# Kernel tuning notes

Measured on AMD Instinct MI355X. Metric: run time of the kernel, lower is better.

## Reference

```python
import jax, jax.numpy as jnp
import numpy as np

B, P, E, D = 256, 2048, 16, 2
HID, OUT = 128, 128
BN_EPS = 1e-5


def setup_inputs() -> dict:
    key = jax.random.key(0)
    ks = jax.random.split(key, 16)
    inp = {
        "barcode_h0": jax.random.normal(ks[0], (B, P, D), jnp.float32),
        "barcode_h0_count": jax.random.randint(ks[1], (B,), 0, P),
        "barcode_h1": jax.random.normal(ks[2], (B, P, D), jnp.float32),
        "barcode_h1_count": jax.random.randint(ks[3], (B,), 0, P),
        # SLayer params (one per homology dim): centers ~ U[0,1), log_sharpness = log(3.0)
        "centers0": jax.random.uniform(ks[4], (E, D), jnp.float32),
        "log_sharp0": jnp.full((E, D), np.log(3.0), jnp.float32),
        "centers1": jax.random.uniform(ks[5], (E, D), jnp.float32),
        "log_sharp1": jnp.full((E, D), np.log(3.0), jnp.float32),
        # head: Linear(2E -> HID, no bias), BN, ReLU, Linear(HID -> OUT, no bias), BN
        "W1": jax.random.normal(ks[6], (2 * E, HID), jnp.float32) / np.sqrt(2 * E),
        "gamma1": jnp.ones((HID,), jnp.float32),
        "beta1": jnp.zeros((HID,), jnp.float32),
        "W2": jax.random.normal(ks[7], (HID, OUT), jnp.float32) / np.sqrt(HID),
        "gamma2": jnp.ones((OUT,), jnp.float32),
        "beta2": jnp.zeros((OUT,), jnp.float32),
    }
    return inp


def _slayer(pts, counts, centers, log_sharp):
    # pts: [B,P,2], counts: [B], centers/log_sharp: [E,2]
    sharp = jax.nn.softplus(log_sharp) + 1e-6                       # [E,2]
    diff = pts[:, :, None, :] - centers[None, None, :, :]           # [B,P,E,2]
    resp = jnp.exp(-jnp.sum(sharp * diff * diff, axis=-1))          # [B,P,E]
    mask = (jnp.arange(pts.shape[1])[None, :] < counts[:, None]).astype(resp.dtype)
    return jnp.sum(resp * mask[:, :, None], axis=1)                 # [B,E]


def _batchnorm_train(x, gamma, beta):
    m = jnp.mean(x, axis=0)
    v = jnp.var(x, axis=0)  # biased, as torch uses for normalization
    return (x - m) * jax.lax.rsqrt(v + BN_EPS) * gamma + beta


def reference(barcode_h0, barcode_h0_count, barcode_h1, barcode_h1_count,
              centers0, log_sharp0, centers1, log_sharp1,
              W1, gamma1, beta1, W2, gamma2, beta2):
    f0 = _slayer(barcode_h0, barcode_h0_count, centers0, log_sharp0)  # [B,E]
    f1 = _slayer(barcode_h1, barcode_h1_count, centers1, log_sharp1)  # [B,E]
    x = jnp.concatenate([f0, f1], axis=1)                             # [B,2E]
    h = jax.nn.relu(_batchnorm_train(x @ W1, gamma1, beta1))          # [B,HID]
    y = _batchnorm_train(h @ W2, gamma2, beta2)                       # [B,OUT]
    norm = jnp.maximum(jnp.linalg.norm(y, axis=1, keepdims=True), 1e-12)
    return y / norm
```

## Files before the change

### kernel.cpp

```cpp
#include <hip/hip_runtime.h>

#define Bsz 256
#define Pn  2048
#define En  16
#define HIDn 128
#define OUTn 128
#define BN_EPS 1e-5f
#define NREP 16
#define NGRP 16
#define POISON_U 0xAAAAAAAAu

typedef unsigned int u32;
typedef unsigned long long u64;


__device__ __forceinline__ float coh_load(const float* p) {
    return __hip_atomic_load(p, __ATOMIC_RELAXED, __HIP_MEMORY_SCOPE_AGENT);
}
__device__ __forceinline__ void coh_store64(u64* p, u64 v) {
    __hip_atomic_store(p, v, __ATOMIC_RELAXED, __HIP_MEMORY_SCOPE_AGENT);
}
__device__ __forceinline__ u64 coh_load64(const u64* p) {
    return __hip_atomic_load(p, __ATOMIC_RELAXED, __HIP_MEMORY_SCOPE_AGENT);
}

__global__ __launch_bounds__(256) void k_fused(
    const float* __restrict__ pts0, const int* __restrict__ cnt0,
    const float* __restrict__ pts1, const int* __restrict__ cnt1,
    const float* __restrict__ c0, const float* __restrict__ ls0,
    const float* __restrict__ c1, const float* __restrict__ ls1,
    const float* __restrict__ W1,
    const float* __restrict__ g1, const float* __restrict__ be1,
    const float* __restrict__ W2,
    const float* __restrict__ g2, const float* __restrict__ be2,
    float* __restrict__ stats,
    u32* __restrict__ bars,
    u64* __restrict__ mstd,
    float* __restrict__ out)
{
    __shared__ float W2ld[HIDn * OUTn];
    __shared__ float4 cs[2][En];
    __shared__ float red[4][32];
    __shared__ float xrow[32];
    __shared__ float hrow[HIDn];
    __shared__ float part[4];
    __shared__ int   amFin;

    const int tid = threadIdx.x;
    const int b   = blockIdx.x;

    float* sum1R   = stats;
    float* sumsq1R = stats + NREP * HIDn;
    float* sum2R   = stats + 2 * NREP * HIDn;
    float* sumsq2R = stats + 3 * NREP * HIDn;
    const int rep = (b & (NREP - 1)) * HIDn;

    u32* leaf0 = bars + (b >> 4) * 64;
    u32* root0 = bars + 1024;
    u32* fin0  = bars + 1088;
    u32* leaf1 = bars + 2048 + (b >> 4) * 64;
    u32* root1 = bars + 3072;
    u32* fin1  = bars + 3136;
    u64* mstd1 = mstd;
    u64* mstd2 = mstd + HIDn;

    if (tid < 32) {
        int h = tid >> 4, e = tid & 15;
        const float* C = h ? c1 : c0;
        const float* L = h ? ls1 : ls0;
        float zx = L[2 * e], zy = L[2 * e + 1];
        float sx = (zx > 20.f) ? zx : logf(1.f + expf(zx));
        float sy = (zy > 20.f) ? zy : logf(1.f + expf(zy));
        cs[h][e] = make_float4(C[2 * e], C[2 * e + 1], sx + 1e-6f, sy + 1e-6f);
    }
    __syncthreads();

    const int n0 = cnt0[b];
    const int n1 = cnt1[b];
    const float4* q0 = (const float4*)(pts0 + (size_t)b * Pn * 2);
    const float4* q1 = (const float4*)(pts1 + (size_t)b * Pn * 2);

    float4 f0[4], f1[4];
    #pragma unroll
    for (int i = 0; i < 4; i++) {
        f0[i] = q0[tid + (i << 8)];
        f1[i] = q1[tid + (i << 8)];
    }
    const float4* W2v = (const float4*)W2;
    float4 w2r[16];
    #pragma unroll
    for (int i = 0; i < 16; i++) w2r[i] = W2v[tid + (i << 8)];

    float g1v = 0.f, b1v = 0.f, g2v = 0.f, b2v = 0.f;
    if (tid < HIDn) { g1v = g1[tid]; b1v = be1[tid]; g2v = g2[tid]; b2v = be2[tid]; }

    float m0a[4], m0b[4], m1a[4], m1b[4];
    #pragma unroll
    for (int i = 0; i < 4; i++) {
        int p = (tid + (i << 8)) << 1;
        m0a[i] = (p     < n0) ? 1.f : 0.f;
        m0b[i] = (p + 1 < n0) ? 1.f : 0.f;
        m1a[i] = (p     < n1) ? 1.f : 0.f;
        m1b[i] = (p + 1 < n1) ? 1.f : 0.f;
    }

    float acc0[En], acc1[En];
    #pragma unroll
    for (int e = 0; e < En; e++) { acc0[e] = 0.f; acc1[e] = 0.f; }

    #pragma unroll
    for (int e = 0; e < En; e++) {
        float4 c = cs[0][e];
        float4 d = cs[1][e];
        float a0 = acc0[e], a1 = acc1[e];
        #pragma unroll
        for (int i = 0; i < 4; i++) {
            float dx, dy;
            dx = f0[i].x - c.x; dy = f0[i].y - c.y;
            a0 = fmaf(m0a[i], __expf(-(c.z * dx * dx + c.w * dy * dy)), a0);
            dx = f0[i].z - c.x; dy = f0[i].w - c.y;
            a0 = fmaf(m0b[i], __expf(-(c.z * dx * dx + c.w * dy * dy)), a0);
            dx = f1[i].x - d.x; dy = f1[i].y - d.y;
            a1 = fmaf(m1a[i], __expf(-(d.z * dx * dx + d.w * dy * dy)), a1);
            dx = f1[i].z - d.x; dy = f1[i].w - d.y;
            a1 = fmaf(m1b[i], __expf(-(d.z * dx * dx + d.w * dy * dy)), a1);
        }
        acc0[e] = a0; acc1[e] = a1;
    }

    #pragma unroll
    for (int i = 0; i < 16; i++)
        ((float4*)W2ld)[tid + (i << 8)] = w2r[i];

    #pragma unroll
    for (int e = 0; e < En; e++) {
        #pragma unroll
        for (int off = 32; off > 0; off >>= 1) {
            acc0[e] += __shfl_down(acc0[e], off, 64);
            acc1[e] += __shfl_down(acc1[e], off, 64);
        }
    }
    const int wave = tid >> 6, lane = tid & 63;
    if (lane == 0) {
        #pragma unroll
        for (int e = 0; e < En; e++) { red[wave][e] = acc0[e]; red[wave][16 + e] = acc1[e]; }
    }
    __syncthreads();
    if (tid < 32) xrow[tid] = red[0][tid] + red[1][tid] + red[2][tid] + red[3][tid];
    __syncthreads();

    float uv = 0.f;
    if (tid < HIDn) {
        #pragma unroll
        for (int k = 0; k < 32; k++) uv = fmaf(xrow[k], W1[k * HIDn + tid], uv);
        atomicAdd(&sum1R[rep + tid], uv);
        atomicAdd(&sumsq1R[rep + tid], uv * uv);
    }

    __syncthreads();
    if (tid == 0) {
        u32 lo = __hip_atomic_fetch_add(leaf0, 1u, __ATOMIC_ACQ_REL, __HIP_MEMORY_SCOPE_AGENT);
        int f = 0;
        if (lo == POISON_U + (Bsz / NGRP - 1)) {
            u32 ro = __hip_atomic_fetch_add(root0, 1u, __ATOMIC_ACQ_REL, __HIP_MEMORY_SCOPE_AGENT);
            f = (ro == POISON_U + (NGRP - 1));
        }
        amFin = f;
    }
    __syncthreads();
    if (amFin) {
        if (tid < HIDn) {
            float s = 0.f, ss = 0.f;
            #pragma unroll
            for (int r = 0; r < NREP; r++) s  += coh_load(&sum1R[r * HIDn + tid]);
            #pragma unroll
            for (int r = 0; r < NREP; r++) ss += coh_load(&sumsq1R[r * HIDn + tid]);
            float m    = s * (1.f / Bsz);
            float var  = ss * (1.f / Bsz) - m * m;
            float A    = rsqrtf(var + BN_EPS) * g1v;
            float Bc   = b1v - m * A;
            coh_store64(&mstd1[tid], (u64)__float_as_uint(A) |
                                     ((u64)__float_as_uint(Bc) << 32));
        }
        __syncthreads();
        if (tid == 0)
            __hip_atomic_fetch_add(fin0, 1u, __ATOMIC_RELEASE, __HIP_MEMORY_SCOPE_AGENT);
    }
    if (tid == 0) {
        while (__hip_atomic_load(fin0, __ATOMIC_RELAXED, __HIP_MEMORY_SCOPE_AGENT)
               != POISON_U + 1u) __builtin_amdgcn_s_sleep(1);
    }
    __syncthreads();

    if (tid < HIDn) {
        u64 pk = coh_load64(&mstd1[tid]);
        float A  = __uint_as_float((u32)pk);
        float Bc = __uint_as_float((u32)(pk >> 32));
        hrow[tid] = fmaxf(fmaf(uv, A, Bc), 0.f);
    }
    __syncthreads();

    float a = 0.f;
    if (tid < OUTn) {
        #pragma unroll 16
        for (int k = 0; k < HIDn; k++) a = fmaf(hrow[k], W2ld[k * OUTn + tid], a);
        atomicAdd(&sum2R[rep + tid], a);
        atomicAdd(&sumsq2R[rep + tid], a * a);
    }

    __syncthreads();
    if (tid == 0) {
        u32 lo = __hip_atomic_fetch_add(leaf1, 1u, __ATOMIC_ACQ_REL, __HIP_MEMORY_SCOPE_AGENT);
        int f = 0;
        if (lo == POISON_U + (Bsz / NGRP - 1)) {
            u32 ro = __hip_atomic_fetch_add(root1, 1u, __ATOMIC_ACQ_REL, __HIP_MEMORY_SCOPE_AGENT);
            f = (ro == POISON_U + (NGRP - 1));
        }
        amFin = f;
    }
    __syncthreads();
    if (amFin) {
        if (tid < HIDn) {
            float s = 0.f, ss = 0.f;
            #pragma unroll
            for (int r = 0; r < NREP; r++) s  += coh_load(&sum2R[r * HIDn + tid]);
            #pragma unroll
            for (int r = 0; r < NREP; r++) ss += coh_load(&sumsq2R[r * HIDn + tid]);
            float m    = s * (1.f / Bsz);
            float var  = ss * (1.f / Bsz) - m * m;
            float A    = rsqrtf(var + BN_EPS) * g2v;
            float Bc   = b2v - m * A;
            coh_store64(&mstd2[tid], (u64)__float_as_uint(A) |
                                     ((u64)__float_as_uint(Bc) << 32));
        }
        __syncthreads();
        if (tid == 0)
            __hip_atomic_fetch_add(fin1, 1u, __ATOMIC_RELEASE, __HIP_MEMORY_SCOPE_AGENT);
    }
    if (tid == 0) {
        while (__hip_atomic_load(fin1, __ATOMIC_RELAXED, __HIP_MEMORY_SCOPE_AGENT)
               != POISON_U + 1u) __builtin_amdgcn_s_sleep(1);
    }
    __syncthreads();

    float y = 0.f;
    if (tid < OUTn) {
        u64 pk = coh_load64(&mstd2[tid]);
        float A  = __uint_as_float((u32)pk);
        float Bc = __uint_as_float((u32)(pk >> 32));
        y = fmaf(a, A, Bc);
    }
    float sq = y * y;
    #pragma unroll
    for (int off = 32; off > 0; off >>= 1) sq += __shfl_down(sq, off, 64);
    if (lane == 0) part[wave] = sq;
    __syncthreads();
    if (tid < OUTn) {
        float total = part[0] + part[1] + part[2] + part[3];
        float norm  = fmaxf(sqrtf(total), 1e-12f);
        out[b * OUTn + tid] = y / norm;
    }
}

extern "C" void kernel_launch(void* const* d_in, const int* in_sizes, int n_in,
                              void* d_out, int out_size, void* d_ws, size_t ws_size,
                              hipStream_t stream) {
    const float* pts0 = (const float*)d_in[0];
    const int*   cnt0 = (const int*)  d_in[1];
    const float* pts1 = (const float*)d_in[2];
    const int*   cnt1 = (const int*)  d_in[3];
    const float* c0   = (const float*)d_in[4];
    const float* ls0  = (const float*)d_in[5];
    const float* c1   = (const float*)d_in[6];
    const float* ls1  = (const float*)d_in[7];
    const float* W1   = (const float*)d_in[8];
    const float* g1   = (const float*)d_in[9];
    const float* be1  = (const float*)d_in[10];
    const float* W2   = (const float*)d_in[11];
    const float* g2   = (const float*)d_in[12];
    const float* be2  = (const float*)d_in[13];
    float* out = (float*)d_out;

    float* stats = (float*)d_ws;
    u32*   bars  = (u32*)((float*)d_ws + 4 * NREP * HIDn);
    u64*   mstd  = (u64*)(bars + 4096);


    k_fused<<<Bsz, 256, 0, stream>>>(pts0, cnt0, pts1, cnt1,
                                     c0, ls0, c1, ls1,
                                     W1, g1, be1, W2, g2, be2,
                                     stats, bars, mstd, out);
}
```

Baseline: 105.7 us.

## Replace atomic BN stat accumulation with per-row stores and distributed leader reductions

Each block now writes its per-row activations to a global matrix instead of atomically adding sums and squared sums into replicated stat buffers. The first 16 blocks act as leaders; each reduces 8 columns over all 256 rows after waiting on the root barrier counter, then publishes its own finish flag. The other blocks poll all 16 flags instead of one counter. This removes atomic contention and the single-block serial finaliser, at the cost of more global traffic, a 16-flag poll, and spin guards that exit silently after a timeout.

```diff
diff --git a/kernel.cpp b/kernel.cpp
--- a/kernel.cpp
+++ b/kernel.cpp
@@ -6,16 +6,26 @@
 #define HIDn 128
 #define OUTn 128
 #define BN_EPS 1e-5f
-#define NREP 16
 #define NGRP 16
 #define POISON_U 0xAAAAAAAAu
+#define FIN_U    0x5A5A5A5Au
+#define SPIN_MAX (1 << 24)
 
 typedef unsigned int u32;
 typedef unsigned long long u64;
 
 
-__device__ __forceinline__ float coh_load(const float* p) {
+__device__ __forceinline__ float coh_loadf(const float* p) {
     return __hip_atomic_load(p, __ATOMIC_RELAXED, __HIP_MEMORY_SCOPE_AGENT);
+}
+__device__ __forceinline__ void coh_storef(float* p, float v) {
+    __hip_atomic_store(p, v, __ATOMIC_RELAXED, __HIP_MEMORY_SCOPE_AGENT);
+}
+__device__ __forceinline__ u32 coh_load32(const u32* p) {
+    return __hip_atomic_load(p, __ATOMIC_RELAXED, __HIP_MEMORY_SCOPE_AGENT);
+}
+__device__ __forceinline__ void coh_store32rel(u32* p, u32 v) {
+    __hip_atomic_store(p, v, __ATOMIC_RELEASE, __HIP_MEMORY_SCOPE_AGENT);
 }
 __device__ __forceinline__ void coh_store64(u64* p, u64 v) {
     __hip_atomic_store(p, v, __ATOMIC_RELAXED, __HIP_MEMORY_SCOPE_AGENT);
@@ -33,7 +43,8 @@
     const float* __restrict__ g1, const float* __restrict__ be1,
     const float* __restrict__ W2,
     const float* __restrict__ g2, const float* __restrict__ be2,
-    float* __restrict__ stats,
+    float* __restrict__ uMat,
+    float* __restrict__ u2Mat,
     u32* __restrict__ bars,
     u64* __restrict__ mstd,
     float* __restrict__ out)
@@ -44,25 +55,25 @@
     __shared__ float xrow[32];
     __shared__ float hrow[HIDn];
     __shared__ float part[4];
-    __shared__ int   amFin;
 
     const int tid = threadIdx.x;
     const int b   = blockIdx.x;
 
-    float* sum1R   = stats;
-    float* sumsq1R = stats + NREP * HIDn;
-    float* sum2R   = stats + 2 * NREP * HIDn;
-    float* sumsq2R = stats + 3 * NREP * HIDn;
-    const int rep = (b & (NREP - 1)) * HIDn;
-
     u32* leaf0 = bars + (b >> 4) * 64;
     u32* root0 = bars + 1024;
-    u32* fin0  = bars + 1088;
     u32* leaf1 = bars + 2048 + (b >> 4) * 64;
     u32* root1 = bars + 3072;
-    u32* fin1  = bars + 3136;
+    u32* fin0  = bars + 4096;
+    u32* fin1  = bars + 4608;
     u64* mstd1 = mstd;
     u64* mstd2 = mstd + HIDn;
+
+    const bool leader = (b < NGRP);
+    const int  col    = (b << 3) + (tid >> 5);
+    const int  bb     = tid & 31;
+
+    float gA1 = 0.f, bA1 = 0.f, gA2 = 0.f, bA2 = 0.f;
+    if (leader) { gA1 = g1[col]; bA1 = be1[col]; gA2 = g2[col]; bA2 = be2[col]; }
 
     if (tid < 32) {
         int h = tid >> 4, e = tid & 15;
@@ -90,9 +101,6 @@
     float4 w2r[16];
     #pragma unroll
     for (int i = 0; i < 16; i++) w2r[i] = W2v[tid + (i << 8)];
-
-    float g1v = 0.f, b1v = 0.f, g2v = 0.f, b2v = 0.f;
-    if (tid < HIDn) { g1v = g1[tid]; b1v = be1[tid]; g2v = g2[tid]; b2v = be2[tid]; }
 
     float m0a[4], m0b[4], m1a[4], m1b[4];
     #pragma unroll
@@ -153,42 +161,57 @@
     if (tid < HIDn) {
         #pragma unroll
         for (int k = 0; k < 32; k++) uv = fmaf(xrow[k], W1[k * HIDn + tid], uv);
-        atomicAdd(&sum1R[rep + tid], uv);
-        atomicAdd(&sumsq1R[rep + tid], uv * uv);
+        coh_storef(&uMat[b * HIDn + tid], uv);
     }
 
     __syncthreads();
     if (tid == 0) {
         u32 lo = __hip_atomic_fetch_add(leaf0, 1u, __ATOMIC_ACQ_REL, __HIP_MEMORY_SCOPE_AGENT);
-        int f = 0;
-        if (lo == POISON_U + (Bsz / NGRP - 1)) {
-            u32 ro = __hip_atomic_fetch_add(root0, 1u, __ATOMIC_ACQ_REL, __HIP_MEMORY_SCOPE_AGENT);
-            f = (ro == POISON_U + (NGRP - 1));
-        }
-        amFin = f;
-    }
-    __syncthreads();
-    if (amFin) {
-        if (tid < HIDn) {
-            float s = 0.f, ss = 0.f;
-            #pragma unroll
-            for (int r = 0; r < NREP; r++) s  += coh_load(&sum1R[r * HIDn + tid]);
-            #pragma unroll
-            for (int r = 0; r < NREP; r++) ss += coh_load(&sumsq1R[r * HIDn + tid]);
+        if (lo == POISON_U + (Bsz / NGRP - 1))
+            __hip_atomic_fetch_add(root0, 1u, __ATOMIC_ACQ_REL, __HIP_MEMORY_SCOPE_AGENT);
+    }
+    if (leader) {
+        if (tid == 0) {
+            int guard = 0;
+            while (coh_load32(root0) != POISON_U + NGRP && ++guard < SPIN_MAX)
+                __builtin_amdgcn_s_sleep(1);
+        }
+        __syncthreads();
+        float v[8];
+        #pragma unroll
+        for (int k = 0; k < 8; k++)
+            v[k] = coh_loadf(&uMat[(bb + (k << 5)) * HIDn + col]);
+        float s = 0.f, ss = 0.f;
+        #pragma unroll
+        for (int k = 0; k < 8; k++) { s += v[k]; ss = fmaf(v[k], v[k], ss); }
+        #pragma unroll
+        for (int off = 16; off > 0; off >>= 1) {
+            s  += __shfl_down(s,  off, 32);
+            ss += __shfl_down(ss, off, 32);
+        }
+        if (bb == 0) {
             float m    = s * (1.f / Bsz);
             float var  = ss * (1.f / Bsz) - m * m;
-            float A    = rsqrtf(var + BN_EPS) * g1v;
-            float Bc   = b1v - m * A;
-            coh_store64(&mstd1[tid], (u64)__float_as_uint(A) |
+            float A    = rsqrtf(var + BN_EPS) * gA1;
+            float Bc   = bA1 - m * A;
+            coh_store64(&mstd1[col], (u64)__float_as_uint(A) |
                                      ((u64)__float_as_uint(Bc) << 32));
         }
         __syncthreads();
-        if (tid == 0)
-            __hip_atomic_fetch_add(fin0, 1u, __ATOMIC_RELEASE, __HIP_MEMORY_SCOPE_AGENT);
+        if (tid == 0) coh_store32rel(&fin0[b * 16], FIN_U);
     }
     if (tid == 0) {
-        while (__hip_atomic_load(fin0, __ATOMIC_RELAXED, __HIP_MEMORY_SCOPE_AGENT)
-               != POISON_U + 1u) __builtin_amdgcn_s_sleep(1);
+        int guard = 0;
+        for (;;) {
+            u32 f[NGRP];
+            #pragma unroll
+            for (int g = 0; g < NGRP; g++) f[g] = coh_load32(&fin0[g * 16]);
+            bool all = true;
+            #pragma unroll
+            for (int g = 0; g < NGRP; g++) all = all && (f[g] != POISON_U);
+            if (all || ++guard >= SPIN_MAX) break;
+            __builtin_amdgcn_s_sleep(2);
+        }
     }
     __syncthreads();
 
@@ -204,42 +227,57 @@
     if (tid < OUTn) {
         #pragma unroll 16
         for (int k = 0; k < HIDn; k++) a = fmaf(hrow[k], W2ld[k * OUTn + tid], a);
-        atomicAdd(&sum2R[rep + tid], a);
-        atomicAdd(&sumsq2R[rep + tid], a * a);
+        coh_storef(&u2Mat[b * OUTn + tid], a);
     }
 
     __syncthreads();
     if (tid == 0) {
         u32 lo = __hip_atomic_fetch_add(leaf1, 1u, __ATOMIC_ACQ_REL, __HIP_MEMORY_SCOPE_AGENT);
-        int f = 0;
-        if (lo == POISON_U + (Bsz / NGRP - 1)) {
-            u32 ro = __hip_atomic_fetch_add(root1, 1u, __ATOMIC_ACQ_REL, __HIP_MEMORY_SCOPE_AGENT);
-            f = (ro == POISON_U + (NGRP - 1));
-        }
-        amFin = f;
-    }
-    __syncthreads();
-    if (amFin) {
-        if (tid < HIDn) {
-            float s = 0.f, ss = 0.f;
-            #pragma unroll
-            for (int r = 0; r < NREP; r++) s  += coh_load(&sum2R[r * HIDn + tid]);
-            #pragma unroll
-            for (int r = 0; r < NREP; r++) ss += coh_load(&sumsq2R[r * HIDn + tid]);
+        if (lo == POISON_U + (Bsz / NGRP - 1))
+            __hip_atomic_fetch_add(root1, 1u, __ATOMIC_ACQ_REL, __HIP_MEMORY_SCOPE_AGENT);
+    }
+    if (leader) {
+        if (tid == 0) {
+            int guard = 0;
+            while (coh_load32(root1) != POISON_U + NGRP && ++guard < SPIN_MAX)
+                __builtin_amdgcn_s_sleep(1);
+        }
+        __syncthreads();
+        float v[8];
+        #pragma unroll
+        for (int k = 0; k < 8; k++)
+            v[k] = coh_loadf(&u2Mat[(bb + (k << 5)) * OUTn + col]);
+        float s = 0.f, ss = 0.f;
+        #pragma unroll
+        for (int k = 0; k < 8; k++) { s += v[k]; ss = fmaf(v[k], v[k], ss); }
+        #pragma unroll
+        for (int off = 16; off > 0; off >>= 1) {
+            s  += __shfl_down(s,  off, 32);
+            ss += __shfl_down(ss, off, 32);
+        }
+        if (bb == 0) {
             float m    = s * (1.f / Bsz);
             float var  = ss * (1.f / Bsz) - m * m;
-            float A    = rsqrtf(var + BN_EPS) * g2v;
-            float Bc   = b2v - m * A;
-            coh_store64(&mstd2[tid], (u64)__float_as_uint(A) |
+            float A    = rsqrtf(var + BN_EPS) * gA2;
+            float Bc   = bA2 - m * A;
+            coh_store64(&mstd2[col], (u64)__float_as_uint(A) |
                                      ((u64)__float_as_uint(Bc) << 32));
         }
         __syncthreads();
-        if (tid == 0)
-            __hip_atomic_fetch_add(fin1, 1u, __ATOMIC_RELEASE, __HIP_MEMORY_SCOPE_AGENT);
+        if (tid == 0) coh_store32rel(&fin1[b * 16], FIN_U);
     }
     if (tid == 0) {
-        while (__hip_atomic_load(fin1, __ATOMIC_RELAXED, __HIP_MEMORY_SCOPE_AGENT)
-               != POISON_U + 1u) __builtin_amdgcn_s_sleep(1);
+        int guard = 0;
+        for (;;) {
+            u32 f[NGRP];
+            #pragma unroll
+            for (int g = 0; g < NGRP; g++) f[g] = coh_load32(&fin1[g * 16]);
+            bool all = true;
+            #pragma unroll
+            for (int g = 0; g < NGRP; g++) all = all && (f[g] != POISON_U);
+            if (all || ++guard >= SPIN_MAX) break;
+            __builtin_amdgcn_s_sleep(2);
+        }
     }
     __syncthreads();
 
@@ -281,13 +319,15 @@
     const float* be2  = (const float*)d_in[13];
     float* out = (float*)d_out;
 
-    float* stats = (float*)d_ws;
-    u32*   bars  = (u32*)((float*)d_ws + 4 * NREP * HIDn);
-    u64*   mstd  = (u64*)(bars + 4096);
+    float* ws    = (float*)d_ws;
+    float* uMat  = ws;
+    float* u2Mat = ws + 32768;
+    u32*   bars  = (u32*)(ws + 65536);
+    u64*   mstd  = (u64*)(bars + 8192);
 
 
     k_fused<<<Bsz, 256, 0, stream>>>(pts0, cnt0, pts1, cnt1,
                                      c0, ls0, c1, ls1,
                                      W1, g1, be1, W2, g2, be2,
-                                     stats, bars, mstd, out);
-}
+                                     uMat, u2Mat, bars, mstd, out);
+}
```

New measurement: 116.4 us. 10.2% more time.
